# Kernel tuning notes

Hardware: AMD Instinct MI355X
Metric: run time of the kernel (lower is better)

## Reference

```python
import jax, jax.numpy as jnp
import numpy as np

B, K = 16384, 32      # batch nodes, sampled neighbors per node
N, F, E = 1000000, 128, 128  # table size, feature_dim, embed_dim


def setup_inputs() -> dict:
    key = jax.random.key(0)
    k1, k2, k3 = jax.random.split(key, 3)
    id2feat = jax.random.normal(k1, (N, F), dtype=jnp.float32)
    # xavier_uniform for weight
    limit = float(np.sqrt(6.0 / (F + E)))
    weight = jax.random.uniform(k2, (F, E), dtype=jnp.float32, minval=-limit, maxval=limit)
    bias = jnp.zeros((E,), dtype=jnp.float32)
    neigh_idx = jax.random.randint(k3, (B, K), 0, N, dtype=jnp.int64)
    return {"id2feat": id2feat, "weight": weight, "bias": bias, "neigh_idx": neigh_idx}


def reference(id2feat, weight, bias, neigh_idx):
    # gather neighbor features: [B, K, F]
    feats = id2feat[neigh_idx]
    # linear transform then mean over neighbors (== mask.mm(embed_matrix))
    emb = jnp.einsum('bkf,fe->bke', feats, weight) + bias  # [B, K, E]
    return emb.mean(axis=1)  # [B, E]
```

## Files before the change

### kernel.cpp

```cpp
#include <hip/hip_runtime.h>


#define BATCH 16384
#define KNB   32
#define FDIM  128
#define EDIM  128
#define ROWS_PER_BLOCK 8
#define IDX_PITCH 33
#define A_PITCH  132

__global__ __launch_bounds__(256, 6)
void spa_agg_kernel(const float* __restrict__ id2feat,
                    const float* __restrict__ weight,
                    const float* __restrict__ bias,
                    const int* __restrict__ neigh_idx,
                    float* __restrict__ out) {
    __shared__ float sA[ROWS_PER_BLOCK * A_PITCH];
    __shared__ int   sIdx[ROWS_PER_BLOCK * IDX_PITCH];

    const int tid = threadIdx.x;
    const int lb  = tid >> 5;
    const int lr  = tid & 31;
    const int b0  = blockIdx.x * ROWS_PER_BLOCK;

    {
        sIdx[lb * IDX_PITCH + lr] = neigh_idx[b0 * KNB + tid];
    }
    __syncthreads();

    {
        float a0 = 0.f, a1 = 0.f, a2 = 0.f, a3 = 0.f;
        const int* ip = &sIdx[lb * IDX_PITCH];
        const float* gbase = id2feat + lr * 4;
        #pragma unroll 8
        for (int k = 0; k < KNB; ++k) {
            const int row = ip[k];
            const float4 r0 = *(const float4*)(gbase + (size_t)row * FDIM);
            a0 += r0.x; a1 += r0.y; a2 += r0.z; a3 += r0.w;
        }
        *(float4*)&sA[lb * A_PITCH + lr * 4] =
            make_float4(a0 * (1.f / 32.f), a1 * (1.f / 32.f),
                        a2 * (1.f / 32.f), a3 * (1.f / 32.f));
    }
    __syncthreads();

    {
        const int e0 = lr * 4;
        float4 acc = *(const float4*)(bias + e0);
        const float* arow = &sA[lb * A_PITCH];
        const float* wp = weight + e0;
        #pragma unroll 8
        for (int f = 0; f < FDIM; ++f) {
            const float a  = arow[f];
            const float4 w = *(const float4*)(wp + (size_t)f * EDIM);
            acc.x += a * w.x; acc.y += a * w.y;
            acc.z += a * w.z; acc.w += a * w.w;
        }
        *(float4*)(out + (size_t)(b0 + lb) * EDIM + e0) = acc;
    }
}

extern "C" void kernel_launch(void* const* d_in, const int* in_sizes, int n_in,
                              void* d_out, int out_size, void* d_ws, size_t ws_size,
                              hipStream_t stream) {
    const float* id2feat = (const float*)d_in[0];
    const float* weight  = (const float*)d_in[1];
    const float* bias    = (const float*)d_in[2];
    const int*   neigh   = (const int*)d_in[3];
    float*       outp    = (float*)d_out;

    dim3 grid(BATCH / ROWS_PER_BLOCK);
    dim3 block(256);
    spa_agg_kernel<<<grid, block, 0, stream>>>(id2feat, weight, bias, neigh, outp);
}
```

Measured before the change: 612.8 us.

## Pipeline neighbor-row gather through LDS with direct global-to-LDS async loads

Replaces the register gather of neighbor feature rows with a ring of 8 in-flight global_load_lds transfers per wave into a shared staging buffer, using explicit vmcnt waits to consume rows as they arrive. Each thread keeps all 32 neighbor indices in registers so the loads can be issued without waiting on LDS index reads. The goal is more outstanding memory requests per wave to hide random-gather latency. In exchange it adds 32KB of LDS for staging and lowers the launch-bounds occupancy hint from 6 to 4, which may cut the number of waves available to hide latency.

```diff
diff --git a/kernel.cpp b/kernel.cpp
--- a/kernel.cpp
+++ b/kernel.cpp
@@ -6,55 +6,88 @@
 #define FDIM  128
 #define EDIM  128
 #define ROWS_PER_BLOCK 8
+#define DEPTH 8
 #define IDX_PITCH 33
 #define A_PITCH  132
 
-__global__ __launch_bounds__(256, 6)
+__global__ __launch_bounds__(256, 4)
 void spa_agg_kernel(const float* __restrict__ id2feat,
                     const float* __restrict__ weight,
                     const float* __restrict__ bias,
                     const int* __restrict__ neigh_idx,
                     float* __restrict__ out) {
-    __shared__ float sA[ROWS_PER_BLOCK * A_PITCH];
-    __shared__ int   sIdx[ROWS_PER_BLOCK * IDX_PITCH];
+    __shared__ float4 stage[4][DEPTH][64];
+    __shared__ float  sA[ROWS_PER_BLOCK * A_PITCH];
+    __shared__ int    sIdx[ROWS_PER_BLOCK * IDX_PITCH];
 
-    const int tid = threadIdx.x;
-    const int lb  = tid >> 5;
-    const int lr  = tid & 31;
-    const int b0  = blockIdx.x * ROWS_PER_BLOCK;
+    const int tid  = threadIdx.x;
+    const int lane = tid & 63;
+    const int wv   = __builtin_amdgcn_readfirstlane(tid >> 6);
+    const int half = lane >> 5;
+    const int lr   = lane & 31;
+    const int b0   = blockIdx.x * ROWS_PER_BLOCK;
 
+    sIdx[(tid >> 5) * IDX_PITCH + (tid & 31)] = neigh_idx[b0 * KNB + tid];
+    __syncthreads();
+
+    int myidx[KNB];
     {
-        sIdx[lb * IDX_PITCH + lr] = neigh_idx[b0 * KNB + tid];
+        const int* ip = &sIdx[(2 * wv + half) * IDX_PITCH];
+        #pragma unroll
+        for (int k = 0; k < KNB; ++k) myidx[k] = ip[k];
     }
+
+    float4* const mybuf = &stage[wv][0][0];
+    const float* gsrc = id2feat + lr * 4;
+
+    #define WAITV(N) asm volatile("s_waitcnt vmcnt(" #N ")" ::: "memory")
+    #define WAITL    asm volatile("s_waitcnt lgkmcnt(0)" ::: "memory")
+
+    #pragma unroll
+    for (int s = 0; s < DEPTH; ++s) {
+        __builtin_amdgcn_global_load_lds(
+            (const void*)(gsrc + (size_t)myidx[s] * FDIM),
+            (void*)(mybuf + s * 64), 16, 0, 0);
+    }
+
+    float a0 = 0.f, a1 = 0.f, a2 = 0.f, a3 = 0.f;
+    #define ACCUM(K) { const float4 v = mybuf[((K) & (DEPTH - 1)) * 64 + lane]; \
+                       a0 += v.x; a1 += v.y; a2 += v.z; a3 += v.w; }
+
+    #pragma unroll
+    for (int k = 0; k < KNB - DEPTH; ++k) {
+        WAITV(7);
+        ACCUM(k);
+        WAITL;
+        __builtin_amdgcn_global_load_lds(
+            (const void*)(gsrc + (size_t)myidx[k + DEPTH] * FDIM),
+            (void*)(mybuf + (k & (DEPTH - 1)) * 64), 16, 0, 0);
+    }
+    WAITV(7); ACCUM(24);
+    WAITV(6); ACCUM(25);
+    WAITV(5); ACCUM(26);
+    WAITV(4); ACCUM(27);
+    WAITV(3); ACCUM(28);
+    WAITV(2); ACCUM(29);
+    WAITV(1); ACCUM(30);
+    WAITV(0); ACCUM(31);
+
+    *(float4*)&sA[(2 * wv + half) * A_PITCH + lr * 4] =
+        make_float4(a0 * (1.f / 32.f), a1 * (1.f / 32.f),
+                    a2 * (1.f / 32.f), a3 * (1.f / 32.f));
     __syncthreads();
 
     {
-        float a0 = 0.f, a1 = 0.f, a2 = 0.f, a3 = 0.f;
-        const int* ip = &sIdx[lb * IDX_PITCH];
-        const float* gbase = id2feat + lr * 4;
-        #pragma unroll 8
-        for (int k = 0; k < KNB; ++k) {
-            const int row = ip[k];
-            const float4 r0 = *(const float4*)(gbase + (size_t)row * FDIM);
-            a0 += r0.x; a1 += r0.y; a2 += r0.z; a3 += r0.w;
-        }
-        *(float4*)&sA[lb * A_PITCH + lr * 4] =
-            make_float4(a0 * (1.f / 32.f), a1 * (1.f / 32.f),
-                        a2 * (1.f / 32.f), a3 * (1.f / 32.f));
-    }
-    __syncthreads();
-
-    {
-        const int e0 = lr * 4;
+        const int lb = tid >> 5;
+        const int e0 = (tid & 31) * 4;
         float4 acc = *(const float4*)(bias + e0);
         const float* arow = &sA[lb * A_PITCH];
-        const float* wp = weight + e0;
         #pragma unroll 8
         for (int f = 0; f < FDIM; ++f) {
             const float a  = arow[f];
-            const float4 w = *(const float4*)(wp + (size_t)f * EDIM);
-            acc.x += a * w.x; acc.y += a * w.y;
-            acc.z += a * w.z; acc.w += a * w.w;
+            const float4 w4 = *(const float4*)(weight + (size_t)f * EDIM + e0);
+            acc.x += a * w4.x; acc.y += a * w4.y;
+            acc.z += a * w4.z; acc.w += a * w4.w;
         }
         *(float4*)(out + (size_t)(b0 + lb) * EDIM + e0) = acc;
     }
```

New measurement: 615.5 us. Within noise of the previous version (+0.4%).
